# Kernel optimization log

Measured on AMD Instinct MI355X. Metric: run time of the kernel, lower is better.

## Reference

```python
import jax, jax.numpy as jnp
import numpy as np

B, C, L = 8, 256, 2048


def setup_inputs() -> dict:
    key = jax.random.key(0)
    ks = jax.random.split(key, 7)
    s = 0.05
    return {
        "x": jax.random.normal(ks[0], (B, C, L), dtype=jnp.float32),
        "Wq": jax.random.normal(ks[1], (C, C), dtype=jnp.float32) * s,
        "bq": jax.random.normal(ks[2], (C,), dtype=jnp.float32) * s,
        "Wk": jax.random.normal(ks[3], (C, C), dtype=jnp.float32) * s,
        "bk": jax.random.normal(ks[4], (C,), dtype=jnp.float32) * s,
        "Wv": jax.random.normal(ks[5], (C, C), dtype=jnp.float32) * s,
        "bv": jax.random.normal(ks[6], (C,), dtype=jnp.float32) * s,
    }


def reference(x, Wq, bq, Wk, bk, Wv, bv):
    # Conv1d with kernel_size=1 == per-position linear over channels.
    # x: [B, C, L]
    scale = x.shape[1] ** (-0.5)
    q = jnp.einsum('oc,bcl->bol', Wq, x) + bq[None, :, None]  # [B,C,L]
    k = jnp.einsum('oc,bcl->bol', Wk, x) + bk[None, :, None]
    v = jnp.einsum('oc,bcl->bol', Wv, x) + bv[None, :, None]
    scores = jnp.einsum('bcl,bcm->blm', q, k) * scale          # [B,L,L]
    attn = jax.nn.softmax(scores, axis=-1)
    context = jnp.einsum('blm,bcm->bcl', attn, v)              # [B,C,L]
    return context + x
```

## Files before the change

kernel.cpp:

```cpp
#include <hip/hip_runtime.h>

#define NB 8
#define NC 256
#define NL 2048
#define SCALE 0.0625f

typedef __attribute__((ext_vector_type(8))) __bf16 bf16x8;
typedef __attribute__((ext_vector_type(4))) float f32x4;
typedef __attribute__((ext_vector_type(4))) unsigned int u32x4;
typedef __attribute__((ext_vector_type(4))) unsigned short u16x4;
typedef __attribute__((ext_vector_type(8))) unsigned short u16x8;

static __device__ __forceinline__ unsigned short f2b(float f) {
    unsigned int u = __builtin_bit_cast(unsigned int, f);
    u += 0x7fffu + ((u >> 16) & 1u);
    return (unsigned short)(u >> 16);
}

__global__ void wconv_kernel(const float* __restrict__ Wq,
                             const float* __restrict__ Wk,
                             const float* __restrict__ Wv,
                             unsigned short* __restrict__ Wbf)
{
    const int fid  = blockIdx.x * 4 + (threadIdx.x >> 6);
    const int lane = threadIdx.x & 63;
    const int mat  = fid >> 7;
    const int oT   = (fid >> 3) & 15;
    const int kt   = fid & 7;
    const float* W = (mat == 0) ? Wq : (mat == 1) ? Wk : Wv;
    const int o = oT * 16 + (lane & 15);
    const int c = kt * 32 + (lane >> 4) * 8;
    float4 a  = *(const float4*)&W[(size_t)o * NC + c];
    float4 b2 = *(const float4*)&W[(size_t)o * NC + c + 4];
    u16x8 p = {f2b(a.x), f2b(a.y), f2b(a.z), f2b(a.w),
               f2b(b2.x), f2b(b2.y), f2b(b2.z), f2b(b2.w)};
    *(u16x8*)&Wbf[(size_t)fid * 512 + lane * 8] = p;
}

__global__ __launch_bounds__(512, 1) void qkv_fused(
    const float* __restrict__ x,
    const unsigned short* __restrict__ Wbf,
    const float* __restrict__ bq, const float* __restrict__ bk,
    const float* __restrict__ bv,
    unsigned short* __restrict__ qT, unsigned short* __restrict__ kT,
    unsigned short* __restrict__ vo)
{
    const int raw = blockIdx.x;
    const int b   = raw & 7;
    const int lt0 = (raw >> 3) * 64;
    const int t    = threadIdx.x;
    const int w    = t >> 6;
    const int lane = t & 63;
    const int ln15 = lane & 15;
    const int quad = lane >> 4;

    __shared__ __align__(16) unsigned short XT[64 * 256];

    {
        const int c  = t >> 1;
        const int hh = t & 1;
        const float* xr = &x[((size_t)(b * NC + c)) * NL + lt0 + hh * 32];
        const int cc = c >> 3, c7 = c & 7;
        #pragma unroll
        for (int j = 0; j < 8; ++j) {
            float4 xv = *(const float4*)&xr[j * 4];
            const int lb = hh * 32 + j * 4;
            unsigned short e0 = f2b(xv.x), e1 = f2b(xv.y),
                           e2 = f2b(xv.z), e3 = f2b(xv.w);
            XT[(lb + 0) * 256 + (cc ^ ((lb + 0) & 15)) * 8 + c7] = e0;
            XT[(lb + 1) * 256 + (cc ^ ((lb + 1) & 15)) * 8 + c7] = e1;
            XT[(lb + 2) * 256 + (cc ^ ((lb + 2) & 15)) * 8 + c7] = e2;
            XT[(lb + 3) * 256 + (cc ^ ((lb + 3) & 15)) * 8 + c7] = e3;
        }
    }
    __syncthreads();

    bf16x8 xf[4][8];
    #pragma unroll
    for (int lt = 0; lt < 4; ++lt) {
        const int l = lt * 16 + ln15;
        #pragma unroll
        for (int kt = 0; kt < 8; ++kt) {
            const int kc = kt * 4 + quad;
            const int pos = kc ^ (l & 15);
            xf[lt][kt] = __builtin_bit_cast(bf16x8, *(const u32x4*)&XT[l * 256 + pos * 8]);
        }
    }

    #pragma unroll
    for (int mat = 0; mat < 3; ++mat) {
        const float* bias = (mat == 0) ? bq : (mat == 1) ? bk : bv;
        #pragma unroll
        for (int ot = 0; ot < 2; ++ot) {
            f32x4 acc[4];
            #pragma unroll
            for (int j = 0; j < 4; ++j) acc[j] = f32x4{0.f, 0.f, 0.f, 0.f};

            const size_t wb = ((size_t)(mat * 16 + w * 2 + ot) * 8) * 512 + lane * 8;
            #pragma unroll
            for (int kt = 0; kt < 8; ++kt) {
                bf16x8 wf = __builtin_bit_cast(bf16x8, *(const u32x4*)&Wbf[wb + (size_t)kt * 512]);
                #pragma unroll
                for (int lt = 0; lt < 4; ++lt)
                    acc[lt] = __builtin_amdgcn_mfma_f32_16x16x32_bf16(wf, xf[lt][kt], acc[lt], 0, 0, 0);
            }

            float bvals[4];
            #pragma unroll
            for (int r = 0; r < 4; ++r)
                bvals[r] = bias[w * 32 + ot * 16 + quad * 4 + r];

            if (mat < 2) {
                unsigned short* out = (mat == 0) ? qT : kT;
                const int o_base = w * 32 + ot * 16 + quad * 4;
                #pragma unroll
                for (int lt = 0; lt < 4; ++lt) {
                    const int l = lt0 + lt * 16 + ln15;
                    u16x4 pk;
                    #pragma unroll
                    for (int r = 0; r < 4; ++r)
                        pk[r] = f2b(acc[lt][r] + bvals[r]);
                    *(u16x4*)&out[((size_t)(b * NL + l)) * NC + o_base] = pk;
                }
            } else {
                #pragma unroll
                for (int lt = 0; lt < 4; ++lt) {
                    const int l = lt0 + lt * 16 + ln15;
                    #pragma unroll
                    for (int r = 0; r < 4; ++r) {
                        const int o = w * 32 + ot * 16 + quad * 4 + r;
                        vo[((size_t)(b * NC + o)) * NL + l] = f2b(acc[lt][r] + bvals[r]);
                    }
                }
            }
        }
    }
}

__global__ __launch_bounds__(512, 1) void attn_kernel(
    const unsigned short* __restrict__ qT,
    const unsigned short* __restrict__ kT,
    const unsigned short* __restrict__ v,
    const float* __restrict__ x,
    float* __restrict__ out)
{
    const int raw  = blockIdx.x;
    const int b    = raw & 7;
    const int l0   = (raw >> 3) * 64;
    const int t    = threadIdx.x;
    const int w    = t >> 6;
    const int lane = t & 63;
    const int ln15 = lane & 15;
    const int quad = lane >> 4;
    const int qg   = w & 3;
    const int kg   = w >> 2;

    __shared__ __align__(16) char smem[139776];
    unsigned short* Kb0 = (unsigned short*)smem;
    unsigned short* Kb1 = (unsigned short*)(smem + 32768);
    unsigned short* Vb0 = (unsigned short*)(smem + 65536);
    unsigned short* Vb1 = (unsigned short*)(smem + 98304);
    unsigned short* Plds = (unsigned short*)(smem + 131072);
    float* denomP = (float*)(smem + 139264);
    float (*ctxbuf)[68] = (float(*)[68])smem;

    bf16x8 qf[8];
    {
        const size_t qrow = ((size_t)b * NL + l0 + qg * 16 + ln15) * NC;
        #pragma unroll
        for (int kt = 0; kt < 8; ++kt)
            qf[kt] = __builtin_bit_cast(bf16x8,
                        *(const u32x4*)&qT[qrow + kt * 32 + quad * 8]);
    }

    f32x4 ctx[16];
    #pragma unroll
    for (int i = 0; i < 16; ++i) ctx[i] = f32x4{0.f, 0.f, 0.f, 0.f};
    float dacc[4] = {0.f, 0.f, 0.f, 0.f};

    auto stage = [&](int mt, unsigned short* Kd, unsigned short* Vd) {
        const int m0 = mt * 64;
        #pragma unroll
        for (int s = 0; s < 4; ++s) {
            const int il = w * 4 + s;
            const int n  = il * 2 + (lane >> 5);
            const int g  = (lane & 31) ^ (n & 15);
            const unsigned short* gp = &kT[((size_t)b * NL + m0 + n) * NC + g * 8];
            __builtin_amdgcn_global_load_lds(
                (const __attribute__((address_space(1))) unsigned int*)gp,
                (__attribute__((address_space(3))) unsigned int*)&Kd[il * 512],
                16, 0, 0);
        }
        #pragma unroll
        for (int s = 0; s < 4; ++s) {
            const int il = w * 4 + s;
            const int c  = il * 8 + (lane >> 3);
            const int g  = (lane & 7) ^ (c & 7);
            const unsigned short* gp = &v[((size_t)(b * NC + c)) * NL + m0 + g * 8];
            __builtin_amdgcn_global_load_lds(
                (const __attribute__((address_space(1))) unsigned int*)gp,
                (__attribute__((address_space(3))) unsigned int*)&Vd[il * 512],
                16, 0, 0);
        }
    };

    stage(0, Kb0, Vb0);
    __syncthreads();

    for (int mt = 0; mt < 32; ++mt) {
        if (mt < 31) {
            if (mt & 1) stage(mt + 1, Kb0, Vb0);
            else        stage(mt + 1, Kb1, Vb1);
        }
        const unsigned short* Kd = (mt & 1) ? Kb1 : Kb0;
        const unsigned short* Vd = (mt & 1) ? Vb1 : Vb0;

        f32x4 sacc[2];
        sacc[0] = f32x4{0.f, 0.f, 0.f, 0.f};
        sacc[1] = f32x4{0.f, 0.f, 0.f, 0.f};
        #pragma unroll
        for (int nt = 0; nt < 2; ++nt) {
            const int n = kg * 32 + nt * 16 + ln15;
            #pragma unroll
            for (int kt = 0; kt < 8; ++kt) {
                const int p = (kt * 4 + quad) ^ ln15;
                bf16x8 bf = __builtin_bit_cast(bf16x8,
                              *(const u32x4*)&Kd[n * 256 + p * 8]);
                sacc[nt] = __builtin_amdgcn_mfma_f32_16x16x32_bf16(
                               qf[kt], bf, sacc[nt], 0, 0, 0);
            }
        }

        float rs[4] = {0.f, 0.f, 0.f, 0.f};
        #pragma unroll
        for (int nt = 0; nt < 2; ++nt) {
            #pragma unroll
            for (int r = 0; r < 4; ++r) {
                float e = __expf(sacc[nt][r] * SCALE);
                rs[r] += e;
                const int ip = qg * 16 + quad * 4 + r;
                const int j  = kg * 32 + nt * 16 + ln15;
                const int pc = (j >> 3) ^ (ip & 7);
                Plds[ip * 64 + pc * 8 + (j & 7)] = f2b(e);
            }
        }
        #pragma unroll
        for (int r = 0; r < 4; ++r) {
            rs[r] += __shfl_xor(rs[r], 1, 64);
            rs[r] += __shfl_xor(rs[r], 2, 64);
            rs[r] += __shfl_xor(rs[r], 4, 64);
            rs[r] += __shfl_xor(rs[r], 8, 64);
            dacc[r] += rs[r];
        }

        bf16x8 pf;
        {
            const int m = qg * 16 + ln15;
            const int p = (kg * 4 + quad) ^ (m & 7);
            pf = __builtin_bit_cast(bf16x8, *(const u32x4*)&Plds[m * 64 + p * 8]);
        }
        #pragma unroll
        for (int ct = 0; ct < 16; ++ct) {
            const int c = ct * 16 + ln15;
            const int p = (kg * 4 + quad) ^ (c & 7);
            bf16x8 vb = __builtin_bit_cast(bf16x8,
                          *(const u32x4*)&Vd[c * 64 + p * 8]);
            ctx[ct] = __builtin_amdgcn_mfma_f32_16x16x32_bf16(
                          pf, vb, ctx[ct], 0, 0, 0);
        }

        __syncthreads();
    }

    if (kg == 1) {
        #pragma unroll
        for (int ct = 0; ct < 16; ++ct) {
            const int c = ct * 16 + ln15;
            #pragma unroll
            for (int r = 0; r < 4; ++r)
                ctxbuf[c][qg * 16 + quad * 4 + r] = ctx[ct][r];
        }
    }
    if (ln15 == 0) {
        #pragma unroll
        for (int r = 0; r < 4; ++r)
            denomP[kg * 64 + qg * 16 + quad * 4 + r] = dacc[r];
    }
    __syncthreads();
    if (kg == 0) {
        float rinv[4];
        #pragma unroll
        for (int r = 0; r < 4; ++r) {
            const int ql = qg * 16 + quad * 4 + r;
            rinv[r] = 1.0f / (denomP[ql] + denomP[64 + ql]);
        }
        #pragma unroll
        for (int ct = 0; ct < 16; ++ct) {
            const int c = ct * 16 + ln15;
            #pragma unroll
            for (int r = 0; r < 4; ++r) {
                const int ql = qg * 16 + quad * 4 + r;
                ctxbuf[c][ql] = (ctx[ct][r] + ctxbuf[c][ql]) * rinv[r];
            }
        }
    }
    __syncthreads();

    #pragma unroll
    for (int p = 0; p < 8; ++p) {
        const int f  = t + 512 * p;
        const int c  = f >> 4;
        const int lg = (f & 15) * 4;
        const size_t idx = ((size_t)(b * NC + c)) * NL + l0 + lg;
        float4 xv = *(const float4*)&x[idx];
        float4 cv = *(const float4*)&ctxbuf[c][lg];
        float4 o = make_float4(cv.x + xv.x, cv.y + xv.y, cv.z + xv.z, cv.w + xv.w);
        *(float4*)&out[idx] = o;
    }
}

extern "C" void kernel_launch(void* const* d_in, const int* in_sizes, int n_in,
                              void* d_out, int out_size, void* d_ws, size_t ws_size,
                              hipStream_t stream) {
    const float* x  = (const float*)d_in[0];
    const float* Wq = (const float*)d_in[1];
    const float* bq = (const float*)d_in[2];
    const float* Wk = (const float*)d_in[3];
    const float* bk = (const float*)d_in[4];
    const float* Wv = (const float*)d_in[5];
    const float* bv = (const float*)d_in[6];
    float* out = (float*)d_out;

    const size_t plane = (size_t)NB * NC * NL;
    unsigned short* qT  = (unsigned short*)d_ws;
    unsigned short* kT  = qT + plane;
    unsigned short* v   = kT + plane;
    unsigned short* Wbf = v + plane;

    wconv_kernel<<<96, 256, 0, stream>>>(Wq, Wk, Wv, Wbf);

    qkv_fused<<<256, 512, 0, stream>>>(x, Wbf, bq, bk, bv, qT, kT, v);

    attn_kernel<<<256, 512, 0, stream>>>(qT, kT, v, x, out);
}
```

Before: 166.0 us.

## Split QKV projection across blocks per matrix and repartition attention warps

The QKV projection kernel now launches three times as many blocks, with each block computing only one of Q, K or V. This adds parallelism across the GPU, at the cost of each block re-loading and transposing its x tile. The attention kernel's warp decomposition changes from 4 query groups × 2 key groups to 2 query groups × 4 key groups. Each warp now computes scores for 32 queries against 16 keys, writes P to LDS, syncs, and accumulates context for a 64-channel slice of V. This removes the cross-warp context reduction through LDS but adds an extra barrier per key tile.

```diff
diff --git a/kernel.cpp b/kernel.cpp
--- a/kernel.cpp
+++ b/kernel.cpp
@@ -47,7 +47,8 @@
 {
     const int raw = blockIdx.x;
     const int b   = raw & 7;
-    const int lt0 = (raw >> 3) * 64;
+    const int lt0 = ((raw >> 3) & 31) * 64;
+    const int mat = raw >> 8;
     const int t    = threadIdx.x;
     const int w    = t >> 6;
     const int lane = t & 63;
@@ -65,12 +66,10 @@
         for (int j = 0; j < 8; ++j) {
             float4 xv = *(const float4*)&xr[j * 4];
             const int lb = hh * 32 + j * 4;
-            unsigned short e0 = f2b(xv.x), e1 = f2b(xv.y),
-                           e2 = f2b(xv.z), e3 = f2b(xv.w);
-            XT[(lb + 0) * 256 + (cc ^ ((lb + 0) & 15)) * 8 + c7] = e0;
-            XT[(lb + 1) * 256 + (cc ^ ((lb + 1) & 15)) * 8 + c7] = e1;
-            XT[(lb + 2) * 256 + (cc ^ ((lb + 2) & 15)) * 8 + c7] = e2;
-            XT[(lb + 3) * 256 + (cc ^ ((lb + 3) & 15)) * 8 + c7] = e3;
+            XT[(lb + 0) * 256 + (cc ^ ((lb + 0) & 15)) * 8 + c7] = f2b(xv.x);
+            XT[(lb + 1) * 256 + (cc ^ ((lb + 1) & 15)) * 8 + c7] = f2b(xv.y);
+            XT[(lb + 2) * 256 + (cc ^ ((lb + 2) & 15)) * 8 + c7] = f2b(xv.z);
+            XT[(lb + 3) * 256 + (cc ^ ((lb + 3) & 15)) * 8 + c7] = f2b(xv.w);
         }
     }
     __syncthreads();
@@ -87,50 +86,47 @@
         }
     }
 
-    #pragma unroll
-    for (int mat = 0; mat < 3; ++mat) {
-        const float* bias = (mat == 0) ? bq : (mat == 1) ? bk : bv;
-        #pragma unroll
-        for (int ot = 0; ot < 2; ++ot) {
-            f32x4 acc[4];
-            #pragma unroll
-            for (int j = 0; j < 4; ++j) acc[j] = f32x4{0.f, 0.f, 0.f, 0.f};
-
-            const size_t wb = ((size_t)(mat * 16 + w * 2 + ot) * 8) * 512 + lane * 8;
-            #pragma unroll
-            for (int kt = 0; kt < 8; ++kt) {
-                bf16x8 wf = __builtin_bit_cast(bf16x8, *(const u32x4*)&Wbf[wb + (size_t)kt * 512]);
+    const float* bias = (mat == 0) ? bq : (mat == 1) ? bk : bv;
+    #pragma unroll
+    for (int ot = 0; ot < 2; ++ot) {
+        f32x4 acc[4];
+        #pragma unroll
+        for (int j = 0; j < 4; ++j) acc[j] = f32x4{0.f, 0.f, 0.f, 0.f};
+
+        const size_t wb = ((size_t)(mat * 16 + w * 2 + ot) * 8) * 512 + lane * 8;
+        #pragma unroll
+        for (int kt = 0; kt < 8; ++kt) {
+            bf16x8 wf = __builtin_bit_cast(bf16x8, *(const u32x4*)&Wbf[wb + (size_t)kt * 512]);
+            #pragma unroll
+            for (int lt = 0; lt < 4; ++lt)
+                acc[lt] = __builtin_amdgcn_mfma_f32_16x16x32_bf16(wf, xf[lt][kt], acc[lt], 0, 0, 0);
+        }
+
+        float bvals[4];
+        #pragma unroll
+        for (int r = 0; r < 4; ++r)
+            bvals[r] = bias[w * 32 + ot * 16 + quad * 4 + r];
+
+        if (mat < 2) {
+            unsigned short* out = (mat == 0) ? qT : kT;
+            const int o_base = w * 32 + ot * 16 + quad * 4;
+            #pragma unroll
+            for (int lt = 0; lt < 4; ++lt) {
+                const int l = lt0 + lt * 16 + ln15;
+                u16x4 pk;
                 #pragma unroll
-                for (int lt = 0; lt < 4; ++lt)
-                    acc[lt] = __builtin_amdgcn_mfma_f32_16x16x32_bf16(wf, xf[lt][kt], acc[lt], 0, 0, 0);
-            }
-
-            float bvals[4];
-            #pragma unroll
-            for (int r = 0; r < 4; ++r)
-                bvals[r] = bias[w * 32 + ot * 16 + quad * 4 + r];
-
-            if (mat < 2) {
-                unsigned short* out = (mat == 0) ? qT : kT;
-                const int o_base = w * 32 + ot * 16 + quad * 4;
+                for (int r = 0; r < 4; ++r)
+                    pk[r] = f2b(acc[lt][r] + bvals[r]);
+                *(u16x4*)&out[((size_t)(b * NL + l)) * NC + o_base] = pk;
+            }
+        } else {
+            #pragma unroll
+            for (int lt = 0; lt < 4; ++lt) {
+                const int l = lt0 + lt * 16 + ln15;
                 #pragma unroll
-                for (int lt = 0; lt < 4; ++lt) {
-                    const int l = lt0 + lt * 16 + ln15;
-                    u16x4 pk;
-                    #pragma unroll
-                    for (int r = 0; r < 4; ++r)
-                        pk[r] = f2b(acc[lt][r] + bvals[r]);
-                    *(u16x4*)&out[((size_t)(b * NL + l)) * NC + o_base] = pk;
-                }
-            } else {
-                #pragma unroll
-                for (int lt = 0; lt < 4; ++lt) {
-                    const int l = lt0 + lt * 16 + ln15;
-                    #pragma unroll
-                    for (int r = 0; r < 4; ++r) {
-                        const int o = w * 32 + ot * 16 + quad * 4 + r;
-                        vo[((size_t)(b * NC + o)) * NL + l] = f2b(acc[lt][r] + bvals[r]);
-                    }
+                for (int r = 0; r < 4; ++r) {
+                    const int o = w * 32 + ot * 16 + quad * 4 + r;
+                    vo[((size_t)(b * NC + o)) * NL + l] = f2b(acc[lt][r] + bvals[r]);
                 }
             }
         }
@@ -152,10 +148,10 @@
     const int lane = t & 63;
     const int ln15 = lane & 15;
     const int quad = lane >> 4;
-    const int qg   = w & 3;
-    const int kg   = w >> 2;
-
-    __shared__ __align__(16) char smem[139776];
+    const int qg   = w & 1;
+    const int kg   = w >> 1;
+
+    __shared__ __align__(16) char smem[140288];
     unsigned short* Kb0 = (unsigned short*)smem;
     unsigned short* Kb1 = (unsigned short*)(smem + 32768);
     unsigned short* Vb0 = (unsigned short*)(smem + 65536);
@@ -164,19 +160,22 @@
     float* denomP = (float*)(smem + 139264);
     float (*ctxbuf)[68] = (float(*)[68])smem;
 
-    bf16x8 qf[8];
-    {
-        const size_t qrow = ((size_t)b * NL + l0 + qg * 16 + ln15) * NC;
+    bf16x8 qf[2][8];
+    #pragma unroll
+    for (int qt = 0; qt < 2; ++qt) {
+        const size_t qrow = ((size_t)b * NL + l0 + qg * 32 + qt * 16 + ln15) * NC;
         #pragma unroll
         for (int kt = 0; kt < 8; ++kt)
-            qf[kt] = __builtin_bit_cast(bf16x8,
-                        *(const u32x4*)&qT[qrow + kt * 32 + quad * 8]);
-    }
-
-    f32x4 ctx[16];
-    #pragma unroll
-    for (int i = 0; i < 16; ++i) ctx[i] = f32x4{0.f, 0.f, 0.f, 0.f};
-    float dacc[4] = {0.f, 0.f, 0.f, 0.f};
+            qf[qt][kt] = __builtin_bit_cast(bf16x8,
+                            *(const u32x4*)&qT[qrow + kt * 32 + quad * 8]);
+    }
+
+    f32x4 ctx[2][4];
+    #pragma unroll
+    for (int i = 0; i < 2; ++i)
+        #pragma unroll
+        for (int j = 0; j < 4; ++j) ctx[i][j] = f32x4{0.f, 0.f, 0.f, 0.f};
+    float dacc[2][4] = {};
 
     auto stage = [&](int mt, unsigned short* Kd, unsigned short* Vd) {
         const int m0 = mt * 64;
@@ -218,91 +217,93 @@
         f32x4 sacc[2];
         sacc[0] = f32x4{0.f, 0.f, 0.f, 0.f};
         sacc[1] = f32x4{0.f, 0.f, 0.f, 0.f};
-        #pragma unroll
-        for (int nt = 0; nt < 2; ++nt) {
-            const int n = kg * 32 + nt * 16 + ln15;
-            #pragma unroll
-            for (int kt = 0; kt < 8; ++kt) {
-                const int p = (kt * 4 + quad) ^ ln15;
-                bf16x8 bf = __builtin_bit_cast(bf16x8,
-                              *(const u32x4*)&Kd[n * 256 + p * 8]);
-                sacc[nt] = __builtin_amdgcn_mfma_f32_16x16x32_bf16(
-                               qf[kt], bf, sacc[nt], 0, 0, 0);
-            }
-        }
-
-        float rs[4] = {0.f, 0.f, 0.f, 0.f};
-        #pragma unroll
-        for (int nt = 0; nt < 2; ++nt) {
+        const int n = kg * 16 + ln15;
+        #pragma unroll
+        for (int kt = 0; kt < 8; ++kt) {
+            const int p = (kt * 4 + quad) ^ ln15;
+            bf16x8 bf = __builtin_bit_cast(bf16x8,
+                          *(const u32x4*)&Kd[n * 256 + p * 8]);
+            sacc[0] = __builtin_amdgcn_mfma_f32_16x16x32_bf16(qf[0][kt], bf, sacc[0], 0, 0, 0);
+            sacc[1] = __builtin_amdgcn_mfma_f32_16x16x32_bf16(qf[1][kt], bf, sacc[1], 0, 0, 0);
+        }
+
+        #pragma unroll
+        for (int qt = 0; qt < 2; ++qt) {
+            float rs[4];
             #pragma unroll
             for (int r = 0; r < 4; ++r) {
-                float e = __expf(sacc[nt][r] * SCALE);
-                rs[r] += e;
-                const int ip = qg * 16 + quad * 4 + r;
-                const int j  = kg * 32 + nt * 16 + ln15;
+                float e = __expf(sacc[qt][r] * SCALE);
+                rs[r] = e;
+                const int ip = qg * 32 + qt * 16 + quad * 4 + r;
+                const int j  = kg * 16 + ln15;
                 const int pc = (j >> 3) ^ (ip & 7);
                 Plds[ip * 64 + pc * 8 + (j & 7)] = f2b(e);
             }
-        }
+            #pragma unroll
+            for (int r = 0; r < 4; ++r) {
+                rs[r] += __shfl_xor(rs[r], 1, 64);
+                rs[r] += __shfl_xor(rs[r], 2, 64);
+                rs[r] += __shfl_xor(rs[r], 4, 64);
+                rs[r] += __shfl_xor(rs[r], 8, 64);
+                dacc[qt][r] += rs[r];
+            }
+        }
+
+        __syncthreads();
+
+        bf16x8 pf[2][2];
+        #pragma unroll
+        for (int qt = 0; qt < 2; ++qt) {
+            const int m = qg * 32 + qt * 16 + ln15;
+            #pragma unroll
+            for (int k2 = 0; k2 < 2; ++k2) {
+                const int p = (k2 * 4 + quad) ^ (m & 7);
+                pf[qt][k2] = __builtin_bit_cast(bf16x8,
+                               *(const u32x4*)&Plds[m * 64 + p * 8]);
+            }
+        }
+        #pragma unroll
+        for (int ct = 0; ct < 4; ++ct) {
+            const int c = kg * 64 + ct * 16 + ln15;
+            #pragma unroll
+            for (int k2 = 0; k2 < 2; ++k2) {
+                const int p = (k2 * 4 + quad) ^ (c & 7);
+                bf16x8 vb = __builtin_bit_cast(bf16x8,
+                              *(const u32x4*)&Vd[c * 64 + p * 8]);
+                ctx[0][ct] = __builtin_amdgcn_mfma_f32_16x16x32_bf16(pf[0][k2], vb, ctx[0][ct], 0, 0, 0);
+                ctx[1][ct] = __builtin_amdgcn_mfma_f32_16x16x32_bf16(pf[1][k2], vb, ctx[1][ct], 0, 0, 0);
+            }
+        }
+
+        __syncthreads();
+    }
+
+    if (ln15 == 0) {
+        #pragma unroll
+        for (int qt = 0; qt < 2; ++qt)
+            #pragma unroll
+            for (int r = 0; r < 4; ++r)
+                denomP[kg * 64 + qg * 32 + qt * 16 + quad * 4 + r] = dacc[qt][r];
+    }
+    __syncthreads();
+    float rinv[2][4];
+    #pragma unroll
+    for (int qt = 0; qt < 2; ++qt)
         #pragma unroll
         for (int r = 0; r < 4; ++r) {
-            rs[r] += __shfl_xor(rs[r], 1, 64);
-            rs[r] += __shfl_xor(rs[r], 2, 64);
-            rs[r] += __shfl_xor(rs[r], 4, 64);
-            rs[r] += __shfl_xor(rs[r], 8, 64);
-            dacc[r] += rs[r];
-        }
-
-        bf16x8 pf;
-        {
-            const int m = qg * 16 + ln15;
-            const int p = (kg * 4 + quad) ^ (m & 7);
-            pf = __builtin_bit_cast(bf16x8, *(const u32x4*)&Plds[m * 64 + p * 8]);
-        }
-        #pragma unroll
-        for (int ct = 0; ct < 16; ++ct) {
-            const int c = ct * 16 + ln15;
-            const int p = (kg * 4 + quad) ^ (c & 7);
-            bf16x8 vb = __builtin_bit_cast(bf16x8,
-                          *(const u32x4*)&Vd[c * 64 + p * 8]);
-            ctx[ct] = __builtin_amdgcn_mfma_f32_16x16x32_bf16(
-                          pf, vb, ctx[ct], 0, 0, 0);
-        }
-
-        __syncthreads();
-    }
-
-    if (kg == 1) {
-        #pragma unroll
-        for (int ct = 0; ct < 16; ++ct) {
-            const int c = ct * 16 + ln15;
+            const int q = qg * 32 + qt * 16 + quad * 4 + r;
+            rinv[qt][r] = 1.0f / (denomP[q] + denomP[64 + q] +
+                                  denomP[128 + q] + denomP[192 + q]);
+        }
+    __syncthreads();
+    #pragma unroll
+    for (int ct = 0; ct < 4; ++ct) {
+        const int c = kg * 64 + ct * 16 + ln15;
+        #pragma unroll
+        for (int qt = 0; qt < 2; ++qt)
             #pragma unroll
             for (int r = 0; r < 4; ++r)
-                ctxbuf[c][qg * 16 + quad * 4 + r] = ctx[ct][r];
-        }
-    }
-    if (ln15 == 0) {
-        #pragma unroll
-        for (int r = 0; r < 4; ++r)
-            denomP[kg * 64 + qg * 16 + quad * 4 + r] = dacc[r];
-    }
-    __syncthreads();
-    if (kg == 0) {
-        float rinv[4];
-        #pragma unroll
-        for (int r = 0; r < 4; ++r) {
-            const int ql = qg * 16 + quad * 4 + r;
-            rinv[r] = 1.0f / (denomP[ql] + denomP[64 + ql]);
-        }
-        #pragma unroll
-        for (int ct = 0; ct < 16; ++ct) {
-            const int c = ct * 16 + ln15;
-            #pragma unroll
-            for (int r = 0; r < 4; ++r) {
-                const int ql = qg * 16 + quad * 4 + r;
-                ctxbuf[c][ql] = (ctx[ct][r] + ctxbuf[c][ql]) * rinv[r];
-            }
-        }
+                ctxbuf[c][qg * 32 + qt * 16 + quad * 4 + r] = ctx[qt][ct][r] * rinv[qt][r];
     }
     __syncthreads();
 
@@ -339,7 +340,7 @@
 
     wconv_kernel<<<96, 256, 0, stream>>>(Wq, Wk, Wv, Wbf);
 
-    qkv_fused<<<256, 512, 0, stream>>>(x, Wbf, bq, bk, bv, qT, kT, v);
+    qkv_fused<<<768, 512, 0, stream>>>(x, Wbf, bq, bk, bv, qT, kT, v);
 
     attn_kernel<<<256, 512, 0, stream>>>(qT, kT, v, x, out);
 }
```

Result: slower. 174.3 us (+5.0%).
